# Performance work log

Hardware: AMD Instinct MI355X
Metric: run time of the kernel (lower is better)

Reference implementation:

```python
import jax, jax.numpy as jnp
import numpy as np

T, B, D = 2048, 16, 1024
DELTA_INIT = -2.0

def _xavier(key, shape, gain=1.0):
    fan_in, fan_out = shape[1], shape[0]
    limit = gain * np.sqrt(6.0 / (fan_in + fan_out))
    return jax.random.uniform(key, shape, jnp.float32, -limit, limit)

def setup_inputs() -> dict:
    key = jax.random.key(0)
    ks = jax.random.split(key, 4)
    return {
        "x": jax.random.normal(ks[0], (T, B, D), jnp.float32),
        "h0": jnp.zeros((B, D), jnp.float32),
        "W_x": _xavier(ks[1], (D, D)),
        "r_h": jnp.zeros((D,), jnp.float32),
        "W_delta": _xavier(ks[2], (D, D), gain=0.1),
        "W_gate": _xavier(ks[3], (D, D)),
        "b": jnp.zeros((D,), jnp.float32),
        "b_delta": jnp.full((D,), DELTA_INIT, jnp.float32),
        "b_gate": jnp.zeros((D,), jnp.float32),
    }

def reference(x, h0, W_x, r_h, W_delta, W_gate, b, b_delta, b_gate):
    # Precompute input projections as batched GEMMs (independent of h):
    delta = jax.nn.sigmoid(jnp.einsum('tbd,ed->tbe', x, W_delta) + b_delta)  # [T,B,D]
    cand_x = jnp.einsum('tbd,ed->tbe', x, W_x) + b                            # [T,B,D]
    gate = jax.nn.silu(jnp.einsum('tbd,ed->tbe', x, W_gate) + b_gate)        # [T,B,D]

    def step(h_prev, inp):
        d_t, cx_t = inp
        cand = jnp.tanh(cx_t + r_h * h_prev)
        h_new = (1.0 - d_t) * h_prev + d_t * cand
        return h_new, h_new

    _, h_seq = jax.lax.scan(step, h0, (delta, cand_x))  # h_seq: [T,B,D]
    output = h_seq * gate
    h = jnp.concatenate([h0[None], h_seq], axis=0)  # [T+1,B,D]
    return output, h
```

## Files before the change

kernel.cpp:

```cpp
#include <hip/hip_runtime.h>
#include <hip/hip_bf16.h>

#define T_DIM 2048
#define B_DIM 16
#define D_DIM 1024
#define M_DIM (T_DIM * B_DIM)
#define K_DIM D_DIM
#define N_DIM (3 * D_DIM)
#define BD (B_DIM * D_DIM)
#define CHUNKS 64
#define CLEN (T_DIM / CHUNKS)
#define NT (K_DIM / 64)

typedef __attribute__((ext_vector_type(8))) short bf16x8;
typedef __attribute__((ext_vector_type(4))) float f32x4;
typedef __attribute__((ext_vector_type(4))) unsigned short us4;
typedef __attribute__((ext_vector_type(8))) unsigned short us8;

__device__ __forceinline__ unsigned short f2bf(float f) {
    unsigned int u = __builtin_bit_cast(unsigned int, f);
    u += 0x7fffu + ((u >> 16) & 1u);
    return (unsigned short)(u >> 16);
}
__device__ __forceinline__ float bf2f(unsigned short s) {
    unsigned int u = ((unsigned int)s) << 16;
    return __builtin_bit_cast(float, u);
}
__device__ __forceinline__ float sigmoid_f(float x) {
    return __builtin_amdgcn_rcpf(1.0f + __expf(-x));
}
__device__ __forceinline__ float tanh_f(float x) {
    float e = __expf(2.0f * x);
    return 1.0f - 2.0f * __builtin_amdgcn_rcpf(e + 1.0f);
}

__device__ __forceinline__ void gload_lds16(const unsigned short* g, unsigned short* l) {
    __builtin_amdgcn_global_load_lds(
        (const __attribute__((address_space(1))) unsigned int*)g,
        (__attribute__((address_space(3))) unsigned int*)l, 16, 0, 0);
}

__device__ __forceinline__ bf16x8 lds_rd(const unsigned short* lds, int slot, int srow, int kk, int lk) {
    int ce = (((kk * 64) + (lk * 16)) ^ ((srow & 7) << 4)) >> 1;
    return *reinterpret_cast<const bf16x8*>(lds + slot * 8192 + srow * 64 + ce);
}

__global__ __launch_bounds__(256)
void conv_bf16(const float* __restrict__ in, unsigned short* __restrict__ outp, int n8)
{
    int i = blockIdx.x * 256 + threadIdx.x;
    if (i >= n8) return;
    const f32x4* p = reinterpret_cast<const f32x4*>(in) + (size_t)i * 2;
    f32x4 v0 = __builtin_nontemporal_load(p);
    f32x4 v1 = __builtin_nontemporal_load(p + 1);
    us8 w;
    w[0] = f2bf(v0[0]); w[1] = f2bf(v0[1]); w[2] = f2bf(v0[2]); w[3] = f2bf(v0[3]);
    w[4] = f2bf(v1[0]); w[5] = f2bf(v1[1]); w[6] = f2bf(v1[2]); w[7] = f2bf(v1[3]);
    *reinterpret_cast<us8*>(outp + (size_t)i * 8) = w;
}

__global__ __launch_bounds__(512, 2)
void gemm_fused(const unsigned short* __restrict__ xb,
                const unsigned short* __restrict__ Wb,
                const float* __restrict__ bx, const float* __restrict__ bdl,
                const float* __restrict__ bg,
                unsigned short* __restrict__ cxw, unsigned short* __restrict__ dw,
                unsigned short* __restrict__ gw)
{
    __shared__ unsigned short lds[8 * 8192];
    unsigned short* ldsA = lds;
    unsigned short* ldsB = lds + 4 * 8192;

    const int NWG = (M_DIM / 256) * (N_DIM / 256);
    int bid = blockIdx.x;
    int wg  = (bid & 7) * (NWG / 8) + (bid >> 3);
    const int bidM = wg / 12;
    const int bidN = wg % 12;
    const int tM  = bidM * 256;
    const int tN  = bidN * 256;
    const int arr = tN >> 10;
    const int nb  = tN & 1023;

    const float* bias = (arr == 0) ? bx : (arr == 1) ? bdl : bg;
    unsigned short* outp = (arr == 0) ? cxw : (arr == 1) ? dw : gw;

    const int tid  = threadIdx.x;
    const int lane = tid & 63;
    const int wid  = tid >> 6;
    const int wr = wid >> 2, wc = wid & 3;
    const int lr = lane & 15, lk = lane >> 4;

    const unsigned short* Asrc = xb + (size_t)tM * K_DIM;
    const unsigned short* Bsrc = Wb + (size_t)arr * (D_DIM * K_DIM) + (size_t)nb * K_DIM;

    const int t8 = tid >> 3;
    const int ke = (((tid & 7) ^ (t8 & 7)) << 3);
    auto arow = [&](int h, int w) {
        int s = w * 64 + t8;
        return ((s >> 4) & 1) * 128 + (h * 4 + (s >> 5)) * 16 + (s & 15);
    };
    const int rA00 = arow(0, 0), rA01 = arow(0, 1);
    const int rA10 = arow(1, 0), rA11 = arow(1, 1);

    auto stA = [&](int t, int r0, int r1, int slot) {
        gload_lds16(Asrc + (size_t)r0 * K_DIM + t * 64 + ke, ldsA + slot * 8192 + wid * 512);
        gload_lds16(Asrc + (size_t)r1 * K_DIM + t * 64 + ke, ldsA + slot * 8192 + 4096 + wid * 512);
    };
    auto stB = [&](int t, int h, int slot) {
        gload_lds16(Bsrc + (size_t)(h * 128 + t8) * K_DIM + t * 64 + ke,      ldsB + slot * 8192 + wid * 512);
        gload_lds16(Bsrc + (size_t)(h * 128 + 64 + t8) * K_DIM + t * 64 + ke, ldsB + slot * 8192 + 4096 + wid * 512);
    };

    f32x4 acc[8][4];
#pragma unroll
    for (int mi = 0; mi < 8; mi++)
#pragma unroll
        for (int ni = 0; ni < 4; ni++)
            acc[mi][ni] = (f32x4){0.f, 0.f, 0.f, 0.f};

    stA(0, rA00, rA01, 0);
    stA(0, rA10, rA11, 1);
    stB(0, 0, 0);
    stB(0, 1, 1);
    stB(1, 0, 2);
    stA(1, rA00, rA01, 2);
    stB(1, 1, 3);
    asm volatile("s_waitcnt vmcnt(6)" ::: "memory");
    __builtin_amdgcn_s_barrier();

    bf16x8 bf[4][2], af[2][2];

#define LOAD_AF(P, ASLOT)                                                          \
    do {                                                                           \
        _Pragma("unroll") for (int j = 0; j < 2; j++)                              \
            _Pragma("unroll") for (int kk = 0; kk < 2; kk++)                       \
                af[j][kk] = lds_rd(ldsA, (ASLOT),                                  \
                                   ((2 * (P) + j) & 3) * 32 + wr * 16 + lr, kk, lk); \
    } while (0)

#define PHASE_MFMA(P)                                                              \
    do {                                                                           \
        __builtin_amdgcn_s_setprio(1);                                             \
        _Pragma("unroll") for (int j = 0; j < 2; j++)                              \
            _Pragma("unroll") for (int ni = 0; ni < 4; ni++) {                     \
                acc[2 * (P) + j][ni] = __builtin_amdgcn_mfma_f32_16x16x32_bf16(    \
                    af[j][0], bf[ni][0], acc[2 * (P) + j][ni], 0, 0, 0);           \
                acc[2 * (P) + j][ni] = __builtin_amdgcn_mfma_f32_16x16x32_bf16(    \
                    af[j][1], bf[ni][1], acc[2 * (P) + j][ni], 0, 0, 0);           \
            }                                                                      \
        __builtin_amdgcn_s_setprio(0);                                             \
    } while (0)

#define WAIT_LGKM()                                          \
    do {                                                     \
        asm volatile("s_waitcnt lgkmcnt(0)" ::: "memory");   \
        __builtin_amdgcn_sched_barrier(0);                   \
    } while (0)

    for (int kt = 0; kt < NT; ++kt) {
        const int par = kt & 1;
        const int a0 = 2 * par, a1 = 2 * par + 1;
        const int bslot = 2 * par + (wc >> 1);
        const int brow  = (wc & 1) * 64;

#pragma unroll
        for (int ni = 0; ni < 4; ni++)
#pragma unroll
            for (int kk = 0; kk < 2; kk++)
                bf[ni][kk] = lds_rd(ldsB, bslot, brow + ni * 16 + lr, kk, lk);
        LOAD_AF(0, a0);
        if (kt + 1 < NT) stA(kt + 1, rA10, rA11, 2 * (1 - par) + 1);
        __builtin_amdgcn_s_barrier();
        WAIT_LGKM();
        PHASE_MFMA(0);
        __builtin_amdgcn_s_barrier();

        LOAD_AF(1, a0);
        if (kt + 2 < NT) stB(kt + 2, 0, 2 * par);
        __builtin_amdgcn_s_barrier();
        WAIT_LGKM();
        PHASE_MFMA(1);
        __builtin_amdgcn_s_barrier();

        LOAD_AF(2, a1);
        if (kt + 2 < NT) stA(kt + 2, rA00, rA01, 2 * par);
        __builtin_amdgcn_s_barrier();
        WAIT_LGKM();
        PHASE_MFMA(2);
        __builtin_amdgcn_s_barrier();

        LOAD_AF(3, a1);
        if (kt + 2 < NT) stB(kt + 2, 1, 2 * par + 1);
        if (kt < NT - 2) asm volatile("s_waitcnt vmcnt(6)" ::: "memory");
        else             asm volatile("s_waitcnt vmcnt(0)" ::: "memory");
        __builtin_amdgcn_s_barrier();
        WAIT_LGKM();
        PHASE_MFMA(3);
        __builtin_amdgcn_s_barrier();
    }

#pragma unroll
    for (int ni = 0; ni < 4; ni++) {
        int lc = wc * 64 + ni * 16 + lr;
        float bia = bias[nb + lc];
#pragma unroll
        for (int mi = 0; mi < 8; mi++) {
            int r0 = wr * 128 + mi * 16 + lk * 4;
#pragma unroll
            for (int r = 0; r < 4; r++) {
                float v = acc[mi][ni][r] + bia;
                if (arr == 1)      v = sigmoid_f(v);
                else if (arr == 2) v = v * sigmoid_f(v);
                int row  = r0 + r;
                int byte = (row * 512 + lc * 2) ^ ((row & 7) << 4);
                *reinterpret_cast<unsigned short*>(
                    reinterpret_cast<char*>(lds) + byte) = f2bf(v);
            }
        }
    }
    __syncthreads();
#pragma unroll
    for (int it = 0; it < 16; ++it) {
        int off8 = it * 512 + tid;
        int row  = off8 >> 5;
        int col8 = (off8 & 31) << 3;
        int byte = (row * 512 + col8 * 2) ^ ((row & 7) << 4);
        us8 v = *reinterpret_cast<const us8*>(reinterpret_cast<char*>(lds) + byte);
        *reinterpret_cast<us8*>(outp + (size_t)(tM + row) * D_DIM + nb + col8) = v;
    }
#undef LOAD_AF
#undef PHASE_MFMA
#undef WAIT_LGKM
}

__global__ __launch_bounds__(256)
void scan_pass1(const unsigned short* __restrict__ dw,
                const unsigned short* __restrict__ cxw,
                float* __restrict__ Aw, float* __restrict__ Bw)
{
    int g  = blockIdx.x * 256 + threadIdx.x;
    int c  = g / (BD / 4);
    int i0 = (g % (BD / 4)) * 4;
    size_t base = (size_t)c * CLEN * BD + i0;

    float a[4]  = {1.f, 1.f, 1.f, 1.f};
    float hb[4] = {0.f, 0.f, 0.f, 0.f};
    for (int t = 0; t < CLEN; t++) {
        us4 dv = *reinterpret_cast<const us4*>(dw  + base + (size_t)t * BD);
        us4 cv = *reinterpret_cast<const us4*>(cxw + base + (size_t)t * BD);
#pragma unroll
        for (int j = 0; j < 4; j++) {
            float d = bf2f(dv[j]);
            float om = 1.f - d;
            float cand = tanh_f(bf2f(cv[j]));
            hb[j] = om * hb[j] + d * cand;
            a[j] *= om;
        }
    }
    f32x4 av = {a[0], a[1], a[2], a[3]};
    f32x4 bv = {hb[0], hb[1], hb[2], hb[3]};
    *reinterpret_cast<f32x4*>(Aw + (size_t)c * BD + i0) = av;
    *reinterpret_cast<f32x4*>(Bw + (size_t)c * BD + i0) = bv;
}

__global__ __launch_bounds__(256)
void scan_pass2(const float* __restrict__ Aw, const float* __restrict__ Bw,
                const float* __restrict__ h0, float* __restrict__ hin,
                float* __restrict__ hseq)
{
    int i0 = (blockIdx.x * 256 + threadIdx.x) * 4;
    if (i0 >= BD) return;
    f32x4 h = *reinterpret_cast<const f32x4*>(h0 + i0);
    *reinterpret_cast<f32x4*>(hseq + i0) = h;
    for (int c = 0; c < CHUNKS; c++) {
        *reinterpret_cast<f32x4*>(hin + (size_t)c * BD + i0) = h;
        f32x4 A  = *reinterpret_cast<const f32x4*>(Aw + (size_t)c * BD + i0);
        f32x4 Bv = *reinterpret_cast<const f32x4*>(Bw + (size_t)c * BD + i0);
        h = A * h + Bv;
    }
}

__global__ __launch_bounds__(256)
void scan_pass3(const unsigned short* __restrict__ dw,
                const unsigned short* __restrict__ cxw,
                const unsigned short* __restrict__ gw,
                const float* __restrict__ hin,
                float* __restrict__ out, float* __restrict__ hseq)
{
    int g  = blockIdx.x * 256 + threadIdx.x;
    int c  = g / (BD / 4);
    int i0 = (g % (BD / 4)) * 4;
    size_t base = (size_t)c * CLEN * BD + i0;

    f32x4 h4 = *reinterpret_cast<const f32x4*>(hin + (size_t)c * BD + i0);
    float h[4] = {h4[0], h4[1], h4[2], h4[3]};
    for (int t = 0; t < CLEN; t++) {
        size_t idx = base + (size_t)t * BD;
        us4 dv = *reinterpret_cast<const us4*>(dw  + idx);
        us4 cv = *reinterpret_cast<const us4*>(cxw + idx);
        us4 gv = *reinterpret_cast<const us4*>(gw  + idx);
        f32x4 o, hv;
#pragma unroll
        for (int j = 0; j < 4; j++) {
            float d = bf2f(dv[j]);
            float om = 1.f - d;
            float cand = tanh_f(bf2f(cv[j]));
            h[j] = om * h[j] + d * cand;
            o[j] = h[j] * bf2f(gv[j]);
            hv[j] = h[j];
        }
        __builtin_nontemporal_store(o,  reinterpret_cast<f32x4*>(out + idx));
        __builtin_nontemporal_store(hv, reinterpret_cast<f32x4*>(hseq + idx + BD));
    }
}

__global__ __launch_bounds__(256)
void scan_fixup(const float* __restrict__ rh, const float* __restrict__ h0,
                const unsigned short* __restrict__ dw,
                const unsigned short* __restrict__ cxw,
                const unsigned short* __restrict__ gw,
                float* __restrict__ out, float* __restrict__ hseq)
{
    int i = blockIdx.x * 256 + threadIdx.x;
    if (i >= BD) return;
    float r = rh[i & (D_DIM - 1)];
    if (r == 0.0f) return;
    float h = h0[i];
    for (int t = 0; t < T_DIM; t++) {
        size_t idx = (size_t)t * BD + i;
        float d = bf2f(dw[idx]);
        float cand = tanh_f(bf2f(cxw[idx]) + r * h);
        h = (1.f - d) * h + d * cand;
        out[idx] = h * bf2f(gw[idx]);
        hseq[idx + BD] = h;
    }
}

extern "C" void kernel_launch(void* const* d_in, const int* in_sizes, int n_in,
                              void* d_out, int out_size, void* d_ws, size_t ws_size,
                              hipStream_t stream)
{
    const float* x   = (const float*)d_in[0];
    const float* h0  = (const float*)d_in[1];
    const float* Wx  = (const float*)d_in[2];
    const float* rh  = (const float*)d_in[3];
    const float* Wd  = (const float*)d_in[4];
    const float* Wg  = (const float*)d_in[5];
    const float* bx  = (const float*)d_in[6];
    const float* bdl = (const float*)d_in[7];
    const float* bg  = (const float*)d_in[8];

    float* out  = (float*)d_out;
    float* hseq = out + (size_t)T_DIM * BD;

    unsigned short* dw  = (unsigned short*)d_ws;
    unsigned short* cxw = dw  + (size_t)M_DIM * D_DIM;
    unsigned short* gw  = cxw + (size_t)M_DIM * D_DIM;
    float* Aw  = (float*)(gw + (size_t)M_DIM * D_DIM);
    float* Bw  = Aw + (size_t)CHUNKS * BD;
    float* hin = Bw + (size_t)CHUNKS * BD;

    unsigned short* xb = (unsigned short*)d_out;
    unsigned short* Wb = xb + (size_t)M_DIM * K_DIM;

    conv_bf16<<<dim3(M_DIM * K_DIM / 8 / 256), dim3(256), 0, stream>>>(x, xb, M_DIM * K_DIM / 8);
    conv_bf16<<<dim3(D_DIM * K_DIM / 8 / 256), dim3(256), 0, stream>>>(Wx, Wb, D_DIM * K_DIM / 8);
    conv_bf16<<<dim3(D_DIM * K_DIM / 8 / 256), dim3(256), 0, stream>>>(Wd, Wb + (size_t)D_DIM * K_DIM, D_DIM * K_DIM / 8);
    conv_bf16<<<dim3(D_DIM * K_DIM / 8 / 256), dim3(256), 0, stream>>>(Wg, Wb + (size_t)2 * D_DIM * K_DIM, D_DIM * K_DIM / 8);

    gemm_fused<<<dim3((M_DIM / 256) * (N_DIM / 256)), dim3(512), 0, stream>>>(
        xb, Wb, bx, bdl, bg, cxw, dw, gw);

    scan_pass1<<<dim3(CHUNKS * BD / 4 / 256), dim3(256), 0, stream>>>(dw, cxw, Aw, Bw);
    scan_pass2<<<dim3(BD / 4 / 256 + 1), dim3(256), 0, stream>>>(Aw, Bw, h0, hin, hseq);
    scan_pass3<<<dim3(CHUNKS * BD / 4 / 256), dim3(256), 0, stream>>>(dw, cxw, gw, hin, out, hseq);
    scan_fixup<<<dim3(BD / 256), dim3(256), 0, stream>>>(rh, h0, dw, cxw, gw, out, hseq);
}
```

Before: 384.5 us.

## Merge bf16 conversion launches and vectorize GEMM epilogue stores

```diff
diff --git a/kernel.cpp b/kernel.cpp
--- a/kernel.cpp
+++ b/kernel.cpp
@@ -45,18 +45,28 @@
     return *reinterpret_cast<const bf16x8*>(lds + slot * 8192 + srow * 64 + ce);
 }
 
-__global__ __launch_bounds__(256)
-void conv_bf16(const float* __restrict__ in, unsigned short* __restrict__ outp, int n8)
+#define XN8 (M_DIM * K_DIM / 8)
+#define WN8 (D_DIM * K_DIM / 8)
+__global__ __launch_bounds__(256)
+void conv_all(const float* __restrict__ x,  const float* __restrict__ Wx,
+              const float* __restrict__ Wd, const float* __restrict__ Wg,
+              unsigned short* __restrict__ xb, unsigned short* __restrict__ Wb)
 {
     int i = blockIdx.x * 256 + threadIdx.x;
-    if (i >= n8) return;
-    const f32x4* p = reinterpret_cast<const f32x4*>(in) + (size_t)i * 2;
+    const float* src;
+    unsigned short* dst;
+    int off;
+    if (i < XN8)                { src = x;  dst = xb;               off = i; }
+    else if (i < XN8 + WN8)     { src = Wx; dst = Wb;               off = i - XN8; }
+    else if (i < XN8 + 2 * WN8) { src = Wd; dst = Wb + (size_t)WN8 * 8;     off = i - XN8 - WN8; }
+    else                        { src = Wg; dst = Wb + (size_t)2 * WN8 * 8; off = i - XN8 - 2 * WN8; }
+    const f32x4* p = reinterpret_cast<const f32x4*>(src) + (size_t)off * 2;
     f32x4 v0 = __builtin_nontemporal_load(p);
     f32x4 v1 = __builtin_nontemporal_load(p + 1);
     us8 w;
     w[0] = f2bf(v0[0]); w[1] = f2bf(v0[1]); w[2] = f2bf(v0[2]); w[3] = f2bf(v0[3]);
     w[4] = f2bf(v1[0]); w[5] = f2bf(v1[1]); w[6] = f2bf(v1[2]); w[7] = f2bf(v1[3]);
-    *reinterpret_cast<us8*>(outp + (size_t)i * 8) = w;
+    *reinterpret_cast<us8*>(dst + (size_t)off * 8) = w;
 }
 
 __global__ __launch_bounds__(512, 2)
@@ -144,9 +154,9 @@
         _Pragma("unroll") for (int j = 0; j < 2; j++)                              \
             _Pragma("unroll") for (int ni = 0; ni < 4; ni++) {                     \
                 acc[2 * (P) + j][ni] = __builtin_amdgcn_mfma_f32_16x16x32_bf16(    \
-                    af[j][0], bf[ni][0], acc[2 * (P) + j][ni], 0, 0, 0);           \
+                    bf[ni][0], af[j][0], acc[2 * (P) + j][ni], 0, 0, 0);           \
                 acc[2 * (P) + j][ni] = __builtin_amdgcn_mfma_f32_16x16x32_bf16(    \
-                    af[j][1], bf[ni][1], acc[2 * (P) + j][ni], 0, 0, 0);           \
+                    bf[ni][1], af[j][1], acc[2 * (P) + j][ni], 0, 0, 0);           \
             }                                                                      \
         __builtin_amdgcn_s_setprio(0);                                             \
     } while (0)
@@ -200,22 +210,22 @@
     }
 
 #pragma unroll
-    for (int ni = 0; ni < 4; ni++) {
-        int lc = wc * 64 + ni * 16 + lr;
-        float bia = bias[nb + lc];
-#pragma unroll
-        for (int mi = 0; mi < 8; mi++) {
-            int r0 = wr * 128 + mi * 16 + lk * 4;
+    for (int mi = 0; mi < 8; mi++) {
+        int row = wr * 128 + mi * 16 + lr;
+#pragma unroll
+        for (int ni = 0; ni < 4; ni++) {
+            int col0 = wc * 64 + ni * 16 + lk * 4;
+            f32x4 bia = *reinterpret_cast<const f32x4*>(bias + nb + col0);
+            us4 w;
 #pragma unroll
             for (int r = 0; r < 4; r++) {
-                float v = acc[mi][ni][r] + bia;
+                float v = acc[mi][ni][r] + bia[r];
                 if (arr == 1)      v = sigmoid_f(v);
                 else if (arr == 2) v = v * sigmoid_f(v);
-                int row  = r0 + r;
-                int byte = (row * 512 + lc * 2) ^ ((row & 7) << 4);
-                *reinterpret_cast<unsigned short*>(
-                    reinterpret_cast<char*>(lds) + byte) = f2bf(v);
+                w[r] = f2bf(v);
             }
+            int byte = (row * 512 + col0 * 2) ^ ((row & 7) << 4);
+            *reinterpret_cast<us4*>(reinterpret_cast<char*>(lds) + byte) = w;
         }
     }
     __syncthreads();
@@ -226,7 +236,8 @@
         int col8 = (off8 & 31) << 3;
         int byte = (row * 512 + col8 * 2) ^ ((row & 7) << 4);
         us8 v = *reinterpret_cast<const us8*>(reinterpret_cast<char*>(lds) + byte);
-        *reinterpret_cast<us8*>(outp + (size_t)(tM + row) * D_DIM + nb + col8) = v;
+        __builtin_nontemporal_store(v,
+            reinterpret_cast<us8*>(outp + (size_t)(tM + row) * D_DIM + nb + col8));
     }
 #undef LOAD_AF
 #undef PHASE_MFMA
@@ -363,10 +374,7 @@
     unsigned short* xb = (unsigned short*)d_out;
     unsigned short* Wb = xb + (size_t)M_DIM * K_DIM;
 
-    conv_bf16<<<dim3(M_DIM * K_DIM / 8 / 256), dim3(256), 0, stream>>>(x, xb, M_DIM * K_DIM / 8);
-    conv_bf16<<<dim3(D_DIM * K_DIM / 8 / 256), dim3(256), 0, stream>>>(Wx, Wb, D_DIM * K_DIM / 8);
-    conv_bf16<<<dim3(D_DIM * K_DIM / 8 / 256), dim3(256), 0, stream>>>(Wd, Wb + (size_t)D_DIM * K_DIM, D_DIM * K_DIM / 8);
-    conv_bf16<<<dim3(D_DIM * K_DIM / 8 / 256), dim3(256), 0, stream>>>(Wg, Wb + (size_t)2 * D_DIM * K_DIM, D_DIM * K_DIM / 8);
+    conv_all<<<dim3((XN8 + 3 * WN8) / 256), dim3(256), 0, stream>>>(x, Wx, Wd, Wg, xb, Wb);
 
     gemm_fused<<<dim3((M_DIM / 256) * (N_DIM / 256)), dim3(512), 0, stream>>>(
         xb, Wb, bx, bdl, bg, cxw, dw, gw);
```

Result: faster. 375.4 us (-2.4%).
